# Performance work log

Hardware: AMD Instinct MI355X
Metric: run time of the kernel (lower is better)

Reference implementation:

```python
import jax, jax.numpy as jnp
import numpy as np

N_NODES = 100000
N_EDGES = 1600000
IN_FEAT = 256
OUT_FEAT = 128


def setup_inputs() -> dict:
    key = jax.random.key(0)
    ks = jax.random.split(key, 8)
    x = jax.random.normal(ks[0], (N_NODES, IN_FEAT), dtype=jnp.float32)
    rows0 = jnp.sort(jax.random.randint(ks[1], (N_EDGES,), 0, N_NODES, dtype=jnp.int32))
    cols0 = jax.random.randint(ks[2], (N_EDGES,), 0, N_NODES, dtype=jnp.int32)
    vals0 = jax.random.uniform(ks[3], (N_EDGES,), dtype=jnp.float32)
    rows1 = jnp.sort(jax.random.randint(ks[4], (N_EDGES,), 0, N_NODES, dtype=jnp.int32))
    cols1 = jax.random.randint(ks[5], (N_EDGES,), 0, N_NODES, dtype=jnp.int32)
    vals1 = jax.random.uniform(ks[6], (N_EDGES,), dtype=jnp.float32)
    kw0, kw1 = jax.random.split(ks[7])
    # glorot-uniform-ish scale for [IN_FEAT, OUT_FEAT]
    limit = float(np.sqrt(6.0 / (IN_FEAT + OUT_FEAT)))
    W0 = jax.random.uniform(kw0, (IN_FEAT, OUT_FEAT), minval=-limit, maxval=limit, dtype=jnp.float32)
    W1 = jax.random.uniform(kw1, (IN_FEAT, OUT_FEAT), minval=-limit, maxval=limit, dtype=jnp.float32)
    return {"x": x, "rows0": rows0, "cols0": cols0, "vals0": vals0,
            "rows1": rows1, "cols1": cols1, "vals1": vals1, "W0": W0, "W1": W1}


def _spmm(rows, cols, vals, dense, n_rows):
    # sparse [N,N] (COO) @ dense [N,D] -> [N,D]
    gathered = vals[:, None] * dense[cols]          # [E, D]
    return jax.ops.segment_sum(gathered, rows, num_segments=n_rows)


def reference(x, rows0, cols0, vals0, rows1, cols1, vals1, W0, W1):
    # GraphConvolution with dropout=0 (identity), featureless=False, no bias, relu.
    # support_i = A_i @ (x @ W_i); output = relu(sum_i support_i)
    s0 = _spmm(rows0, cols0, vals0, x @ W0, N_NODES)
    s1 = _spmm(rows1, cols1, vals1, x @ W1, N_NODES)
    return jax.nn.relu(s0 + s1)
```

## Files before the change

### kernel.cpp

```cpp
#include <hip/hip_runtime.h>
#include <hip/hip_bf16.h>
#include <stdint.h>

#define NN   100000
#define NE   1600000
#define KIN  256
#define FOUT 128

typedef __attribute__((ext_vector_type(8))) short short8;
typedef __attribute__((ext_vector_type(4))) float f32x4;
typedef __attribute__((ext_vector_type(2))) float f32x2;

static __device__ __forceinline__ unsigned short f2bf(float f) {
  unsigned int u = __float_as_uint(f);
  u += 0x7fffu + ((u >> 16) & 1u);
  return (unsigned short)(u >> 16);
}

static __device__ __forceinline__ short8 pack8(float4 u, float4 v) {
  short8 r;
  r[0] = (short)f2bf(u.x); r[1] = (short)f2bf(u.y);
  r[2] = (short)f2bf(u.z); r[3] = (short)f2bf(u.w);
  r[4] = (short)f2bf(v.x); r[5] = (short)f2bf(v.y);
  r[6] = (short)f2bf(v.z); r[7] = (short)f2bf(v.w);
  return r;
}

__global__ void convert_w(const float* __restrict__ W0, const float* __restrict__ W1,
                          unsigned short* __restrict__ wt) {
  int n = blockIdx.x;
  int k = threadIdx.x;
  int which = blockIdx.y;
  const float* W = which ? W1 : W0;
  wt[(size_t)which * (FOUT * KIN) + n * KIN + k] = f2bf(W[k * FOUT + n]);
}

__global__ __launch_bounds__(256) void build_rowptr(const int* __restrict__ rows0,
                                                    const int* __restrict__ rows1,
                                                    int* __restrict__ rp0,
                                                    int* __restrict__ rp1) {
  const int e = blockIdx.x * 256 + threadIdx.x;
  const int* rows = blockIdx.y ? rows1 : rows0;
  int* rp = blockIdx.y ? rp1 : rp0;
  int r1 = rows[e];
  int r2 = (e + 1 < NE) ? rows[e + 1] : NN;
  if (e == 0)
    for (int r = 0; r <= r1; ++r) rp[r] = 0;
  for (int r = r1 + 1; r <= r2; ++r) rp[r] = e + 1;
}

__global__ __launch_bounds__(256) void gemm_mfma(const float* __restrict__ x,
                                                 const unsigned short* __restrict__ wt,
                                                 unsigned short* __restrict__ h) {
  __shared__ __align__(16) unsigned short tile[4][32 * 64];

  const int tid  = threadIdx.x;
  const int lane = tid & 63;
  const int wv   = tid >> 6;
  const int which = blockIdx.y;
  const int rowbase = blockIdx.x * 64 + (wv >> 1) * 32;
  const int colbase = (wv & 1) * 64;
  const int m    = lane & 15;
  const int quad = lane >> 4;

  const unsigned short* w = wt + (size_t)which * (FOUT * KIN);
  unsigned short* hh = h + (size_t)which * NN * FOUT;

  int r0 = rowbase + m;
  int r1 = rowbase + 16 + m;
  int r0c = r0 < NN ? r0 : NN - 1;
  int r1c = r1 < NN ? r1 : NN - 1;
  const float* ap0 = x + (size_t)r0c * KIN + quad * 8;
  const float* ap1 = x + (size_t)r1c * KIN + quad * 8;
  const unsigned short* b0p = w + (size_t)(colbase + 0  + m) * KIN + quad * 8;
  const unsigned short* b1p = w + (size_t)(colbase + 16 + m) * KIN + quad * 8;
  const unsigned short* b2p = w + (size_t)(colbase + 32 + m) * KIN + quad * 8;
  const unsigned short* b3p = w + (size_t)(colbase + 48 + m) * KIN + quad * 8;

  f32x4 acc[2][4];
#pragma unroll
  for (int i = 0; i < 2; ++i)
#pragma unroll
    for (int j = 0; j < 4; ++j)
      acc[i][j] = (f32x4){0.f, 0.f, 0.f, 0.f};

#pragma unroll 2
  for (int ko = 0; ko < KIN; ko += 32) {
    float4 a0lo = *(const float4*)(ap0 + ko);
    float4 a0hi = *(const float4*)(ap0 + ko + 4);
    float4 a1lo = *(const float4*)(ap1 + ko);
    float4 a1hi = *(const float4*)(ap1 + ko + 4);
    short8 b0 = *(const short8*)(b0p + ko);
    short8 b1 = *(const short8*)(b1p + ko);
    short8 b2 = *(const short8*)(b2p + ko);
    short8 b3 = *(const short8*)(b3p + ko);
    short8 a0 = pack8(a0lo, a0hi);
    short8 a1 = pack8(a1lo, a1hi);
    acc[0][0] = __builtin_amdgcn_mfma_f32_16x16x32_bf16(a0, b0, acc[0][0], 0, 0, 0);
    acc[0][1] = __builtin_amdgcn_mfma_f32_16x16x32_bf16(a0, b1, acc[0][1], 0, 0, 0);
    acc[0][2] = __builtin_amdgcn_mfma_f32_16x16x32_bf16(a0, b2, acc[0][2], 0, 0, 0);
    acc[0][3] = __builtin_amdgcn_mfma_f32_16x16x32_bf16(a0, b3, acc[0][3], 0, 0, 0);
    acc[1][0] = __builtin_amdgcn_mfma_f32_16x16x32_bf16(a1, b0, acc[1][0], 0, 0, 0);
    acc[1][1] = __builtin_amdgcn_mfma_f32_16x16x32_bf16(a1, b1, acc[1][1], 0, 0, 0);
    acc[1][2] = __builtin_amdgcn_mfma_f32_16x16x32_bf16(a1, b2, acc[1][2], 0, 0, 0);
    acc[1][3] = __builtin_amdgcn_mfma_f32_16x16x32_bf16(a1, b3, acc[1][3], 0, 0, 0);
  }

#pragma unroll
  for (int i = 0; i < 2; ++i)
#pragma unroll
    for (int reg = 0; reg < 4; ++reg)
#pragma unroll
      for (int j = 0; j < 4; ++j)
        tile[wv][(i * 16 + quad * 4 + reg) * 64 + j * 16 + m] = f2bf(acc[i][j][reg]);

#pragma unroll
  for (int p = 0; p < 4; ++p) {
    int row = p * 8 + (lane >> 3);
    int colb = (lane & 7) * 8;
    uint4 v = *(const uint4*)&tile[wv][row * 64 + colb];
    int grow = rowbase + row;
    if (grow < NN)
      *(uint4*)&hh[(size_t)grow * FOUT + colbase + colb] = v;
  }
}

static __device__ __forceinline__ void consume8(const float* __restrict__ vals, int i,
                                                const unsigned* g, float& sx, float& sy) {
#pragma unroll
  for (int u = 0; u < 8; ++u) {
    float v = vals[i + u];
    sx += v * __uint_as_float(g[u] << 16);
    sy += v * __uint_as_float(g[u] & 0xffff0000u);
  }
}

static __device__ __forceinline__ void tail_spmm(const int* __restrict__ cols,
                                                 const float* __restrict__ vals,
                                                 const unsigned short* __restrict__ hsrc,
                                                 int i, int e, int fo,
                                                 float& sx, float& sy) {
  for (; i + 4 <= e; i += 4) {
    int c0 = cols[i], c1 = cols[i + 1], c2 = cols[i + 2], c3 = cols[i + 3];
    unsigned g0 = *(const unsigned*)(hsrc + (size_t)c0 * FOUT + fo);
    unsigned g1 = *(const unsigned*)(hsrc + (size_t)c1 * FOUT + fo);
    unsigned g2 = *(const unsigned*)(hsrc + (size_t)c2 * FOUT + fo);
    unsigned g3 = *(const unsigned*)(hsrc + (size_t)c3 * FOUT + fo);
    float v0 = vals[i], v1 = vals[i + 1], v2 = vals[i + 2], v3 = vals[i + 3];
    sx += v0 * __uint_as_float(g0 << 16);
    sy += v0 * __uint_as_float(g0 & 0xffff0000u);
    sx += v1 * __uint_as_float(g1 << 16);
    sy += v1 * __uint_as_float(g1 & 0xffff0000u);
    sx += v2 * __uint_as_float(g2 << 16);
    sy += v2 * __uint_as_float(g2 & 0xffff0000u);
    sx += v3 * __uint_as_float(g3 << 16);
    sy += v3 * __uint_as_float(g3 & 0xffff0000u);
  }
  for (; i < e; ++i) {
    int c = cols[i];
    float v = vals[i];
    unsigned g = *(const unsigned*)(hsrc + (size_t)c * FOUT + fo);
    sx += v * __uint_as_float(g << 16);
    sy += v * __uint_as_float(g & 0xffff0000u);
  }
}

__global__ __launch_bounds__(256) void spmm_relu(
    const int* __restrict__ rp0, const int* __restrict__ cols0, const float* __restrict__ vals0,
    const int* __restrict__ rp1, const int* __restrict__ cols1, const float* __restrict__ vals1,
    const unsigned short* __restrict__ h, float* __restrict__ out) {
  const int lane = threadIdx.x & 63;
  int r = blockIdx.x * 4 + (threadIdx.x >> 6);
  r = __builtin_amdgcn_readfirstlane(r);
  const int fo = lane * 2;

  const unsigned short* h0 = h;
  const unsigned short* h1 = h + (size_t)NN * FOUT;

  int i0 = __builtin_amdgcn_readfirstlane(rp0[r]);
  int e0 = __builtin_amdgcn_readfirstlane(rp0[r + 1]);
  int i1 = __builtin_amdgcn_readfirstlane(rp1[r]);
  int e1 = __builtin_amdgcn_readfirstlane(rp1[r + 1]);

  float sx = 0.f, sy = 0.f;

  while (i0 + 8 <= e0 && i1 + 8 <= e1) {
    unsigned g0[8], g1[8];
#pragma unroll
    for (int u = 0; u < 8; ++u) {
      int c = cols0[i0 + u];
      g0[u] = *(const unsigned*)(h0 + (size_t)c * FOUT + fo);
    }
#pragma unroll
    for (int u = 0; u < 8; ++u) {
      int c = cols1[i1 + u];
      g1[u] = *(const unsigned*)(h1 + (size_t)c * FOUT + fo);
    }
    consume8(vals0, i0, g0, sx, sy);
    consume8(vals1, i1, g1, sx, sy);
    i0 += 8;
    i1 += 8;
  }
  tail_spmm(cols0, vals0, h0, i0, e0, fo, sx, sy);
  tail_spmm(cols1, vals1, h1, i1, e1, fo, sx, sy);

  f32x2 o;
  o.x = sx > 0.f ? sx : 0.f;
  o.y = sy > 0.f ? sy : 0.f;
  __builtin_nontemporal_store(o, (f32x2*)(out + (size_t)r * FOUT + fo));
}

extern "C" void kernel_launch(void* const* d_in, const int* in_sizes, int n_in,
                              void* d_out, int out_size, void* d_ws, size_t ws_size,
                              hipStream_t stream) {
  const float* x     = (const float*)d_in[0];
  const int*   rows0 = (const int*)d_in[1];
  const int*   cols0 = (const int*)d_in[2];
  const float* vals0 = (const float*)d_in[3];
  const int*   rows1 = (const int*)d_in[4];
  const int*   cols1 = (const int*)d_in[5];
  const float* vals1 = (const float*)d_in[6];
  const float* W0    = (const float*)d_in[7];
  const float* W1    = (const float*)d_in[8];
  float* out = (float*)d_out;

  char* ws = (char*)d_ws;
  unsigned short* wt = (unsigned short*)(ws);
  unsigned short* h  = (unsigned short*)(ws + 131072);
  int* rp0 = (int*)(ws + 51331072);
  int* rp1 = (int*)(ws + 51731136);

  build_rowptr<<<dim3(6250, 2), 256, 0, stream>>>(rows0, rows1, rp0, rp1);
  convert_w<<<dim3(128, 2), 256, 0, stream>>>(W0, W1, wt);
  gemm_mfma<<<dim3((NN + 63) / 64, 2), 256, 0, stream>>>(x, wt, h);
  spmm_relu<<<25000, 256, 0, stream>>>(rp0, cols0, vals0, rp1, cols1, vals1, h, out);
}
```

Before: 386.6 us.

## Fuse both weight GEMMs into one pass so x is read once

The GEMM kernel now computes x@W0 and x@W1 together in a single launch. Each wave owns 16 rows and all 256 output columns across both weights, so each row of x is loaded and converted to bf16 once instead of twice. This halves x traffic (about 100MB of fp32) but raises accumulator register use to 64 floats per lane plus more B loads per wave, which may lower occupancy.

After: 410.7 us. +6.2%, slower.

```diff
diff --git a/kernel.cpp b/kernel.cpp
--- a/kernel.cpp
+++ b/kernel.cpp
@@ -49,79 +49,64 @@
   for (int r = r1 + 1; r <= r2; ++r) rp[r] = e + 1;
 }
 
-__global__ __launch_bounds__(256) void gemm_mfma(const float* __restrict__ x,
-                                                 const unsigned short* __restrict__ wt,
-                                                 unsigned short* __restrict__ h) {
-  __shared__ __align__(16) unsigned short tile[4][32 * 64];
+__global__ __launch_bounds__(256) void gemm_fused(const float* __restrict__ x,
+                                                  const unsigned short* __restrict__ wt,
+                                                  unsigned short* __restrict__ h) {
+  __shared__ __align__(16) unsigned short tile[4][2][16 * 128];
 
   const int tid  = threadIdx.x;
   const int lane = tid & 63;
   const int wv   = tid >> 6;
-  const int which = blockIdx.y;
-  const int rowbase = blockIdx.x * 64 + (wv >> 1) * 32;
-  const int colbase = (wv & 1) * 64;
   const int m    = lane & 15;
   const int quad = lane >> 4;
-
-  const unsigned short* w = wt + (size_t)which * (FOUT * KIN);
-  unsigned short* hh = h + (size_t)which * NN * FOUT;
-
-  int r0 = rowbase + m;
-  int r1 = rowbase + 16 + m;
-  int r0c = r0 < NN ? r0 : NN - 1;
-  int r1c = r1 < NN ? r1 : NN - 1;
-  const float* ap0 = x + (size_t)r0c * KIN + quad * 8;
-  const float* ap1 = x + (size_t)r1c * KIN + quad * 8;
-  const unsigned short* b0p = w + (size_t)(colbase + 0  + m) * KIN + quad * 8;
-  const unsigned short* b1p = w + (size_t)(colbase + 16 + m) * KIN + quad * 8;
-  const unsigned short* b2p = w + (size_t)(colbase + 32 + m) * KIN + quad * 8;
-  const unsigned short* b3p = w + (size_t)(colbase + 48 + m) * KIN + quad * 8;
-
-  f32x4 acc[2][4];
-#pragma unroll
-  for (int i = 0; i < 2; ++i)
-#pragma unroll
-    for (int j = 0; j < 4; ++j)
-      acc[i][j] = (f32x4){0.f, 0.f, 0.f, 0.f};
+  const int rowbase = blockIdx.x * 64 + wv * 16;
+
+  int r  = rowbase + m;
+  int rc = r < NN ? r : NN - 1;
+  const float* ap = x + (size_t)rc * KIN + quad * 8;
+  const unsigned short* bp = wt + (size_t)m * KIN + quad * 8;
+
+  f32x4 acc0[8], acc1[8];
+#pragma unroll
+  for (int n = 0; n < 8; ++n) {
+    acc0[n] = (f32x4){0.f, 0.f, 0.f, 0.f};
+    acc1[n] = (f32x4){0.f, 0.f, 0.f, 0.f};
+  }
 
 #pragma unroll 2
   for (int ko = 0; ko < KIN; ko += 32) {
-    float4 a0lo = *(const float4*)(ap0 + ko);
-    float4 a0hi = *(const float4*)(ap0 + ko + 4);
-    float4 a1lo = *(const float4*)(ap1 + ko);
-    float4 a1hi = *(const float4*)(ap1 + ko + 4);
-    short8 b0 = *(const short8*)(b0p + ko);
-    short8 b1 = *(const short8*)(b1p + ko);
-    short8 b2 = *(const short8*)(b2p + ko);
-    short8 b3 = *(const short8*)(b3p + ko);
-    short8 a0 = pack8(a0lo, a0hi);
-    short8 a1 = pack8(a1lo, a1hi);
-    acc[0][0] = __builtin_amdgcn_mfma_f32_16x16x32_bf16(a0, b0, acc[0][0], 0, 0, 0);
-    acc[0][1] = __builtin_amdgcn_mfma_f32_16x16x32_bf16(a0, b1, acc[0][1], 0, 0, 0);
-    acc[0][2] = __builtin_amdgcn_mfma_f32_16x16x32_bf16(a0, b2, acc[0][2], 0, 0, 0);
-    acc[0][3] = __builtin_amdgcn_mfma_f32_16x16x32_bf16(a0, b3, acc[0][3], 0, 0, 0);
-    acc[1][0] = __builtin_amdgcn_mfma_f32_16x16x32_bf16(a1, b0, acc[1][0], 0, 0, 0);
-    acc[1][1] = __builtin_amdgcn_mfma_f32_16x16x32_bf16(a1, b1, acc[1][1], 0, 0, 0);
-    acc[1][2] = __builtin_amdgcn_mfma_f32_16x16x32_bf16(a1, b2, acc[1][2], 0, 0, 0);
-    acc[1][3] = __builtin_amdgcn_mfma_f32_16x16x32_bf16(a1, b3, acc[1][3], 0, 0, 0);
-  }
-
-#pragma unroll
-  for (int i = 0; i < 2; ++i)
-#pragma unroll
-    for (int reg = 0; reg < 4; ++reg)
-#pragma unroll
-      for (int j = 0; j < 4; ++j)
-        tile[wv][(i * 16 + quad * 4 + reg) * 64 + j * 16 + m] = f2bf(acc[i][j][reg]);
-
-#pragma unroll
-  for (int p = 0; p < 4; ++p) {
-    int row = p * 8 + (lane >> 3);
-    int colb = (lane & 7) * 8;
-    uint4 v = *(const uint4*)&tile[wv][row * 64 + colb];
-    int grow = rowbase + row;
-    if (grow < NN)
-      *(uint4*)&hh[(size_t)grow * FOUT + colbase + colb] = v;
+    float4 alo = *(const float4*)(ap + ko);
+    float4 ahi = *(const float4*)(ap + ko + 4);
+    short8 a = pack8(alo, ahi);
+#pragma unroll
+    for (int n = 0; n < 8; ++n) {
+      short8 b0 = *(const short8*)(bp + (size_t)(n * 16) * KIN + ko);
+      short8 b1 = *(const short8*)(bp + (size_t)(FOUT + n * 16) * KIN + ko);
+      acc0[n] = __builtin_amdgcn_mfma_f32_16x16x32_bf16(a, b0, acc0[n], 0, 0, 0);
+      acc1[n] = __builtin_amdgcn_mfma_f32_16x16x32_bf16(a, b1, acc1[n], 0, 0, 0);
+    }
+  }
+
+#pragma unroll
+  for (int n = 0; n < 8; ++n)
+#pragma unroll
+    for (int reg = 0; reg < 4; ++reg) {
+      tile[wv][0][(quad * 4 + reg) * 128 + n * 16 + m] = f2bf(acc0[n][reg]);
+      tile[wv][1][(quad * 4 + reg) * 128 + n * 16 + m] = f2bf(acc1[n][reg]);
+    }
+
+#pragma unroll
+  for (int t = 0; t < 2; ++t) {
+    unsigned short* hh = h + (size_t)t * NN * FOUT;
+#pragma unroll
+    for (int p = 0; p < 4; ++p) {
+      int row  = p * 4 + quad;
+      int colb = m * 8;
+      uint4 v = *(const uint4*)&tile[wv][t][row * 128 + colb];
+      int grow = rowbase + row;
+      if (grow < NN)
+        *(uint4*)&hh[(size_t)grow * FOUT + colb] = v;
+    }
   }
 }
 
@@ -232,6 +217,6 @@
 
   build_rowptr<<<dim3(6250, 2), 256, 0, stream>>>(rows0, rows1, rp0, rp1);
   convert_w<<<dim3(128, 2), 256, 0, stream>>>(W0, W1, wt);
-  gemm_mfma<<<dim3((NN + 63) / 64, 2), 256, 0, stream>>>(x, wt, h);
+  gemm_fused<<<dim3((NN + 63) / 64, 1), 256, 0, stream>>>(x, wt, h);
   spmm_relu<<<25000, 256, 0, stream>>>(rp0, cols0, vals0, rp1, cols1, vals1, h, out);
 }
```
